# Kernel tuning notes

Hardware: AMD Instinct MI355X
Metric: run time of the kernel (lower is better)

The kernel has to match this reference:

```python
import jax, jax.numpy as jnp
import numpy as np

EPS = 1e-5
K = 9
DILATION = 1

def bn(x, g, b, m, v):
    # x: (B,C,N,1), inference-mode BatchNorm2d with running stats
    sh = (1, -1, 1, 1)
    return (x - m.reshape(sh)) * (g.reshape(sh) / jnp.sqrt(v.reshape(sh) + EPS)) + b.reshape(sh)

def conv1x1(x, w, b):
    # w: (Cout, Cin), x: (B,Cin,N,1)
    return jnp.einsum('oc,bcnj->bonj', w, x) + b.reshape(1, -1, 1, 1)

def knn_idx(feat, k):
    # feat: (B,C,N) -> (B,N,k) indices of k nearest nodes (incl. self)
    xt = jnp.transpose(feat, (0, 2, 1))  # (B,N,C)
    x2 = jnp.sum(xt * xt, axis=-1)       # (B,N)
    dist = x2[:, :, None] - 2.0 * jnp.einsum('bnc,bmc->bnm', xt, xt) + x2[:, None, :]
    _, idx = jax.lax.top_k(-dist, k)
    return idx

def setup_inputs():
    key = jax.random.key(0)
    ks = jax.random.split(key, 24)
    B, C, H, W = 16, 256, 32, 32
    HID = 512
    def g(i, shape, s=1.0):
        return jax.random.normal(ks[i], shape, dtype=jnp.float32) * s
    def pos(i, shape):
        return jax.random.uniform(ks[i], shape, dtype=jnp.float32, minval=0.5, maxval=1.5)
    return {
        'x': g(0, (B, C, H, W)),
        'fc1_w': g(1, (C, C), 0.05), 'fc1_b': g(2, (C,), 0.05),
        'bn1_g': pos(3, (C,)), 'bn1_b': g(4, (C,), 0.1), 'bn1_m': g(5, (C,), 0.1), 'bn1_v': pos(6, (C,)),
        'gc_w': g(7, (HID, 2 * C), 0.05), 'gc_b': g(8, (HID,), 0.05),
        'gbn_g': pos(9, (HID,)), 'gbn_b': g(10, (HID,), 0.1), 'gbn_m': g(11, (HID,), 0.1), 'gbn_v': pos(12, (HID,)),
        'bn2_g': pos(13, (HID,)), 'bn2_b': g(14, (HID,), 0.1), 'bn2_m': g(15, (HID,), 0.1), 'bn2_v': pos(16, (HID,)),
        'fc2_w': g(17, (C, HID), 0.05), 'fc2_b': g(18, (C,), 0.05),
        'bn3_g': pos(19, (C,)), 'bn3_b': g(20, (C,), 0.1), 'bn3_m': g(21, (C,), 0.1), 'bn3_v': pos(22, (C,)),
    }

def reference(x, fc1_w, fc1_b, bn1_g, bn1_b, bn1_m, bn1_v,
              gc_w, gc_b, gbn_g, gbn_b, gbn_m, gbn_v,
              bn2_g, bn2_b, bn2_m, bn2_v,
              fc2_w, fc2_b, bn3_g, bn3_b, bn3_m, bn3_v):
    B, C, H, W = x.shape
    N = H * W
    x = x.reshape(B, C, N, 1)
    shortcut = x
    # fc1: 1x1 conv + BN
    h = bn(conv1x1(x, fc1_w, fc1_b), bn1_g, bn1_b, bn1_m, bn1_v)
    # DyGraphConv2d: dynamic dilated kNN graph over N nodes
    feat = h[..., 0]  # (B,C,N)
    idx = knn_idx(feat, K * DILATION)[:, :, ::DILATION]  # (B,N,K)
    # MRConv2d: max over neighbors of (x_j - x_i)
    x_j = jax.vmap(lambda f, i: f[:, i])(feat, idx)        # (B,C,N,K) gather
    diff_max = jnp.max(x_j - feat[:, :, :, None], axis=-1)  # (B,C,N)
    # interleave [x, max_diff] along channel dim -> (B, 2C, N, 1)
    m = jnp.stack([feat, diff_max], axis=2).reshape(B, 2 * C, N, 1)
    g = conv1x1(m, gc_w, gc_b)
    g = bn(g, gbn_g, gbn_b, gbn_m, gbn_v)  # BasicConv BN, act='None'
    # graph_conv Sequential: BN + GELU (erf, torch default)
    g = jax.nn.gelu(bn(g, bn2_g, bn2_b, bn2_m, bn2_v), approximate=False)
    # fc2 + residual (drop_path=0 -> identity)
    out = bn(conv1x1(g, fc2_w, fc2_b), bn3_g, bn3_b, bn3_m, bn3_v)
    return out + shortcut
```

## Files before the change

kernel.cpp:

```cpp
#include <hip/hip_runtime.h>
#include <hip/hip_bf16.h>
#include <stdint.h>

typedef unsigned long long u64;
typedef __hip_bfloat16 bf16;
typedef short s8v __attribute__((ext_vector_type(8)));
typedef short s4v __attribute__((ext_vector_type(4)));
typedef float f4v __attribute__((ext_vector_type(4)));

#define B_   16
#define C_   256
#define N_   1024
#define HID_ 512

__device__ __forceinline__ unsigned short f2b(float f) {
    unsigned u = __float_as_uint(f);
    unsigned r = (u + 0x7FFFu + ((u >> 16) & 1u)) >> 16;
    return (unsigned short)r;
}
__device__ __forceinline__ float b2f(unsigned short s) {
    return __uint_as_float(((unsigned)s) << 16);
}
__device__ __forceinline__ float ldIn(const void* p, long long i, int bf) {
    return bf ? b2f(((const unsigned short*)p)[i]) : ((const float*)p)[i];
}

__global__ void prep_kernel(const void* xp,
    const void* fc1_b, const void* bn1_g, const void* bn1_b, const void* bn1_m, const void* bn1_v,
    const void* gc_b,  const void* gbn_g, const void* gbn_b, const void* gbn_m, const void* gbn_v,
    const void* bn2_g, const void* bn2_b, const void* bn2_m, const void* bn2_v,
    const void* fc2_b, const void* bn3_g, const void* bn3_b, const void* bn3_m, const void* bn3_v,
    int* flags, float* s1, float* t1, float* Sg, float* Tg, float* s3, float* t3)
{
    __shared__ int sf;
    if (threadIdx.x == 0) {
        const unsigned short* u = (const unsigned short*)xp;
        int cnt = 0;
        for (int i = 0; i < 64; ++i) {
            int e = (u[2 * i] >> 7) & 0xFF;
            cnt += (e >= 87 && e <= 167);
        }
        int f = (cnt >= 48) ? 1 : 0;
        flags[0] = f;
        sf = f;
    }
    __syncthreads();
    int bf = sf;
    int i = threadIdx.x;
    if (i < 256) {
        float g = ldIn(bn1_g, i, bf), bb = ldIn(bn1_b, i, bf);
        float m = ldIn(bn1_m, i, bf), v  = ldIn(bn1_v, i, bf);
        float s = g / sqrtf(v + 1e-5f);
        s1[i] = s;
        t1[i] = (ldIn(fc1_b, i, bf) - m) * s + bb;

        float g3 = ldIn(bn3_g, i, bf), b3 = ldIn(bn3_b, i, bf);
        float m3 = ldIn(bn3_m, i, bf), v3 = ldIn(bn3_v, i, bf);
        float ss3 = g3 / sqrtf(v3 + 1e-5f);
        s3[i] = ss3;
        t3[i] = (ldIn(fc2_b, i, bf) - m3) * ss3 + b3;
    }
    if (i < 512) {
        float gg = ldIn(gbn_g, i, bf), gb = ldIn(gbn_b, i, bf);
        float gm = ldIn(gbn_m, i, bf), gv = ldIn(gbn_v, i, bf);
        float sg = gg / sqrtf(gv + 1e-5f);
        float g2 = ldIn(bn2_g, i, bf), b2 = ldIn(bn2_b, i, bf);
        float m2 = ldIn(bn2_m, i, bf), v2 = ldIn(bn2_v, i, bf);
        float s2 = g2 / sqrtf(v2 + 1e-5f);
        Sg[i] = sg * s2;
        Tg[i] = ((ldIn(gc_b, i, bf) - gm) * sg + gb - m2) * s2 + b2;
    }
}

__global__ __launch_bounds__(256)
void cast_weights(const void* w1, const void* wg, const void* w2,
                  short* W1b, short* Wgb, short* W2b, const int* flags)
{
    int inf = flags[0];
    int i = blockIdx.x * 256 + threadIdx.x;
    if (i < 65536) {
        W1b[i] = (short)f2b(ldIn(w1, i, inf));
    } else if (i < 65536 + 262144) {
        int j = i - 65536;
        Wgb[j] = (short)f2b(ldIn(wg, j, inf));
    } else {
        int j = i - 327680;
        W2b[j] = (short)f2b(ldIn(w2, j, inf));
    }
}

__global__ __launch_bounds__(256)
void fc1_valu(const void* __restrict__ Aw, const void* __restrict__ Bx,
              float* __restrict__ Ft, const float* __restrict__ s1,
              const float* __restrict__ t1, const int* __restrict__ flags)
{
    __shared__ float As[16][68];
    __shared__ float Bs[16][68];

    int inf = flags[0];
    int b  = blockIdx.z;
    int o0 = blockIdx.y * 64, n0 = blockIdx.x * 64;
    int t  = threadIdx.x;
    int tn = t & 15, to = t >> 4;
    long long bbase = (long long)b * C_ * N_;

    float acc[4][4] = {};

    for (int k0 = 0; k0 < C_; k0 += 16) {
        {
            int l = t * 4;
            int ao = l >> 4, ak = l & 15;
            long long ai = (long long)(o0 + ao) * C_ + k0 + ak;
            As[ak + 0][ao] = ldIn(Aw, ai + 0, inf);
            As[ak + 1][ao] = ldIn(Aw, ai + 1, inf);
            As[ak + 2][ao] = ldIn(Aw, ai + 2, inf);
            As[ak + 3][ao] = ldIn(Aw, ai + 3, inf);
        }
        {
            int l = t * 4;
            int bk = l >> 6, bn = l & 63;
            long long bi = bbase + (long long)(k0 + bk) * N_ + n0 + bn;
            Bs[bk][bn + 0] = ldIn(Bx, bi + 0, inf);
            Bs[bk][bn + 1] = ldIn(Bx, bi + 1, inf);
            Bs[bk][bn + 2] = ldIn(Bx, bi + 2, inf);
            Bs[bk][bn + 3] = ldIn(Bx, bi + 3, inf);
        }
        __syncthreads();
        #pragma unroll
        for (int k = 0; k < 16; ++k) {
            float av[4], bv[4];
            #pragma unroll
            for (int i = 0; i < 4; ++i) av[i] = As[k][to * 4 + i];
            #pragma unroll
            for (int j = 0; j < 4; ++j) bv[j] = Bs[k][tn * 4 + j];
            #pragma unroll
            for (int i = 0; i < 4; ++i)
                #pragma unroll
                for (int j = 0; j < 4; ++j) acc[i][j] += av[i] * bv[j];
        }
        __syncthreads();
    }

    #pragma unroll
    for (int i = 0; i < 4; ++i) {
        int o = o0 + to * 4 + i;
        float s = s1[o], tt = t1[o];
        #pragma unroll
        for (int j = 0; j < 4; ++j) {
            int n = n0 + tn * 4 + j;
            Ft[((long long)(b << 10) + n) * C_ + o] = acc[i][j] * s + tt;
        }
    }
}

__global__ __launch_bounds__(256)
void prep_F(const float* __restrict__ Ft, short* __restrict__ Fhi,
            short* __restrict__ Flo, float* __restrict__ x2)
{
    int t = threadIdx.x;
    int wv = t >> 6, lane = t & 63;
    int n = blockIdx.x * 4 + wv;
    int b = blockIdx.y;
    long long base = ((long long)(b << 10) + n) * C_ + lane * 4;
    f4v f = *(const f4v*)(Ft + base);

    s4v hi, lo;
    #pragma unroll
    for (int r = 0; r < 4; ++r) {
        unsigned short h = f2b(f[r]);
        hi[r] = (short)h;
        lo[r] = (short)f2b(f[r] - b2f(h));
    }
    *(s4v*)(Fhi + base) = hi;
    *(s4v*)(Flo + base) = lo;

    float ss = f[0]*f[0] + f[1]*f[1] + f[2]*f[2] + f[3]*f[3];
    #pragma unroll
    for (int s = 32; s >= 1; s >>= 1) ss += __shfl_xor(ss, s, 64);
    if (lane == 0) x2[(b << 10) + n] = ss;
}

__global__ __launch_bounds__(256)
void gram_topk(const short* __restrict__ Fhi, const short* __restrict__ Flo,
               const float* __restrict__ x2, u64* __restrict__ Part)
{
    __shared__ __align__(16) char ldsbuf[37632];
    short* Ah = (short*)(ldsbuf);
    short* Al = (short*)(ldsbuf + 5120);
    short* Bh = (short*)(ldsbuf + 10240);
    short* Bl = (short*)(ldsbuf + 15360);
    float* Dt = (float*)(ldsbuf + 20480);
    u64*   mrg  = (u64*)(ldsbuf);
    u64*   mrg2 = (u64*)(ldsbuf + 20480);

    int t = threadIdx.x;
    int q0 = blockIdx.x * 64, mq = blockIdx.y, b = blockIdx.z;
    int wv = t >> 6, ln = t & 15, quad = (t >> 4) & 3;
    int wq = (wv & 1) * 32, wm = (wv >> 1) * 32;

    u64 l[9];
    #pragma unroll
    for (int i = 0; i < 9; ++i) l[i] = ~0ULL;

    for (int mt = 0; mt < 4; ++mt) {
        int m0 = mq * 256 + mt * 64;
        f4v acc[2][2];
        #pragma unroll
        for (int i = 0; i < 2; ++i)
            #pragma unroll
            for (int j = 0; j < 2; ++j) acc[i][j] = 0.f;

        for (int kc = 0; kc < 8; ++kc) {
            __syncthreads();
            {
                int row = t >> 2, seg = t & 3;
                long long ga = ((long long)((b << 10) + q0 + row)) * C_ + kc * 32 + seg * 8;
                *(s8v*)&Ah[row * 40 + seg * 8] = *(const s8v*)(Fhi + ga);
                *(s8v*)&Al[row * 40 + seg * 8] = *(const s8v*)(Flo + ga);
                long long gb = ((long long)((b << 10) + m0 + row)) * C_ + kc * 32 + seg * 8;
                *(s8v*)&Bh[row * 40 + seg * 8] = *(const s8v*)(Fhi + gb);
                *(s8v*)&Bl[row * 40 + seg * 8] = *(const s8v*)(Flo + gb);
            }
            __syncthreads();
            s8v ah[2], al[2], bh[2], bl[2];
            #pragma unroll
            for (int i = 0; i < 2; ++i) {
                ah[i] = *(s8v*)&Ah[(wq + i * 16 + ln) * 40 + quad * 8];
                al[i] = *(s8v*)&Al[(wq + i * 16 + ln) * 40 + quad * 8];
            }
            #pragma unroll
            for (int j = 0; j < 2; ++j) {
                bh[j] = *(s8v*)&Bh[(wm + j * 16 + ln) * 40 + quad * 8];
                bl[j] = *(s8v*)&Bl[(wm + j * 16 + ln) * 40 + quad * 8];
            }
            #pragma unroll
            for (int i = 0; i < 2; ++i)
                #pragma unroll
                for (int j = 0; j < 2; ++j) {
                    acc[i][j] = __builtin_amdgcn_mfma_f32_16x16x32_bf16(ah[i], bh[j], acc[i][j], 0, 0, 0);
                    acc[i][j] = __builtin_amdgcn_mfma_f32_16x16x32_bf16(ah[i], bl[j], acc[i][j], 0, 0, 0);
                    acc[i][j] = __builtin_amdgcn_mfma_f32_16x16x32_bf16(al[i], bh[j], acc[i][j], 0, 0, 0);
                    acc[i][j] = __builtin_amdgcn_mfma_f32_16x16x32_bf16(al[i], bl[j], acc[i][j], 0, 0, 0);
                }
        }
        __syncthreads();
        #pragma unroll
        for (int j = 0; j < 2; ++j) {
            int ml = wm + j * 16 + ln;
            float xm = x2[(b << 10) + m0 + ml];
            #pragma unroll
            for (int i = 0; i < 2; ++i) {
                #pragma unroll
                for (int r = 0; r < 4; ++r)
                    Dt[(wq + i * 16 + quad * 4 + r) * 67 + ml] = xm - 2.f * acc[i][j][r];
            }
        }
        __syncthreads();
        {
            int row = t >> 2, part = t & 3;
            #pragma unroll
            for (int c = 0; c < 16; ++c) {
                int cc = part * 16 + c;
                float d = Dt[row * 67 + cc];
                int m = m0 + cc;
                unsigned u = __float_as_uint(d);
                u = (u & 0x80000000u) ? ~u : (u | 0x80000000u);
                u64 key = ((u64)u << 32) | (unsigned)m;
                if (key < l[8]) {
                    u64 x = key;
                    #pragma unroll
                    for (int jj = 0; jj < 9; ++jj) {
                        u64 lo2 = l[jj] < x ? l[jj] : x;
                        u64 hi2 = l[jj] < x ? x : l[jj];
                        l[jj] = lo2; x = hi2;
                    }
                }
            }
        }
    }

    __syncthreads();
    {
        int row = t >> 2, part = t & 3;
        #pragma unroll
        for (int k = 0; k < 9; ++k) mrg[(row * 4 + part) * 9 + k] = l[k];
    }
    __syncthreads();
    if (t < 128) {
        int r = t >> 1, pr = t & 1;
        const u64* LA = &mrg[(r * 4 + pr * 2) * 9];
        const u64* LB = LA + 9;
        int ia = 0, ib = 0;
        u64* Po = &mrg2[(r * 2 + pr) * 9];
        #pragma unroll
        for (int k = 0; k < 9; ++k) {
            u64 va = LA[ia], vb = LB[ib];
            bool ta = va < vb;
            Po[k] = ta ? va : vb;
            ia += ta; ib += !ta;
        }
    }
    __syncthreads();
    if (t < 64) {
        const u64* LA = &mrg2[(t * 2) * 9];
        const u64* LB = LA + 9;
        int ia = 0, ib = 0;
        u64* P = Part + (((long long)((b << 10) + q0 + t)) * 4 + mq) * 9;
        #pragma unroll
        for (int k = 0; k < 9; ++k) {
            u64 va = LA[ia], vb = LB[ib];
            bool ta = va < vb;
            P[k] = ta ? va : vb;
            ia += ta; ib += !ta;
        }
    }
}

__global__ __launch_bounds__(256)
void merge_final(const u64* __restrict__ Part, int* __restrict__ ix)
{
    int row = blockIdx.x * 256 + threadIdx.x;
    const u64* L = Part + (long long)row * 36;
    int p0 = 0, p1 = 0, p2 = 0, p3 = 0;
    #pragma unroll
    for (int k = 0; k < 9; ++k) {
        u64 v0 = L[p0], v1 = L[9 + p1], v2 = L[18 + p2], v3 = L[27 + p3];
        u64 m01 = v0 < v1 ? v0 : v1;
        u64 m23 = v2 < v3 ? v2 : v3;
        u64 mn  = m01 < m23 ? m01 : m23;
        ix[row * 9 + k] = (int)(mn & 0xFFFFFFFFu);
        p0 += (mn == v0);
        p1 += (mn == v1) & (mn != v0);
        p2 += (mn == v2) & (mn != v0) & (mn != v1);
        p3 += (mn == v3) & (mn != v0) & (mn != v1) & (mn != v2);
    }
}

__global__ __launch_bounds__(256)
void build_Mt(const float* __restrict__ Ft, const int* __restrict__ idx,
              short* __restrict__ Mt)
{
    int t = threadIdx.x;
    int wv = t >> 6, lane = t & 63;
    int n = blockIdx.x * 4 + wv;
    int b = blockIdx.y;
    int c0 = lane * 4;
    long long nb = (long long)(b << 10) + n;

    f4v f = *(const f4v*)(Ft + nb * C_ + c0);
    const int* id = idx + nb * 9;
    f4v mx = {-3.4e38f, -3.4e38f, -3.4e38f, -3.4e38f};
    #pragma unroll
    for (int k = 0; k < 9; ++k) {
        f4v g = *(const f4v*)(Ft + ((long long)(b << 10) + id[k]) * C_ + c0);
        mx[0] = fmaxf(mx[0], g[0]); mx[1] = fmaxf(mx[1], g[1]);
        mx[2] = fmaxf(mx[2], g[2]); mx[3] = fmaxf(mx[3], g[3]);
    }
    s8v m8;
    #pragma unroll
    for (int r = 0; r < 4; ++r) {
        m8[2 * r]     = (short)f2b(f[r]);
        m8[2 * r + 1] = (short)f2b(mx[r] - f[r]);
    }
    *(s8v*)(Mt + nb * (2 * C_) + 2 * c0) = m8;
}

template<int EPI>
__global__ __launch_bounds__(256)
void mfma_gemm(const short* __restrict__ A, const short* __restrict__ Bm,
               void* __restrict__ Out, const float* __restrict__ scale,
               const float* __restrict__ bias, const void* __restrict__ resid,
               const int* __restrict__ flags, int K, int Odim)
{
    __shared__ short As[128][40];
    __shared__ short Bs[128][40];

    int t = threadIdx.x, b = blockIdx.z;
    int n0 = blockIdx.x * 128, o0 = blockIdx.y * 128;
    int wv = t >> 6, ln = t & 15, quad = (t >> 4) & 3;
    int wo = (wv & 1) * 64, wn = (wv >> 1) * 64;

    f4v acc[4][4];
    #pragma unroll
    for (int i = 0; i < 4; ++i)
        #pragma unroll
        for (int j = 0; j < 4; ++j) acc[i][j] = 0.f;

    const short* Ab = A + (long long)o0 * K;
    const short* Bb = Bm + ((long long)(b << 10) + n0) * K;

    for (int k0 = 0; k0 < K; k0 += 32) {
        __syncthreads();
        #pragma unroll
        for (int s = 0; s < 2; ++s) {
            int sid = t + s * 256;
            int row = sid >> 2, seg = sid & 3;
            *(s8v*)&As[row][seg * 8] = *(const s8v*)(Ab + (long long)row * K + k0 + seg * 8);
            *(s8v*)&Bs[row][seg * 8] = *(const s8v*)(Bb + (long long)row * K + k0 + seg * 8);
        }
        __syncthreads();
        s8v a[4], bf[4];
        #pragma unroll
        for (int i = 0; i < 4; ++i) a[i]  = *(s8v*)&As[wo + i * 16 + ln][quad * 8];
        #pragma unroll
        for (int j = 0; j < 4; ++j) bf[j] = *(s8v*)&Bs[wn + j * 16 + ln][quad * 8];
        #pragma unroll
        for (int i = 0; i < 4; ++i)
            #pragma unroll
            for (int j = 0; j < 4; ++j)
                acc[i][j] = __builtin_amdgcn_mfma_f32_16x16x32_bf16(a[i], bf[j], acc[i][j], 0, 0, 0);
    }

    int inf = flags[0];
    #pragma unroll
    for (int i = 0; i < 4; ++i) {
        int ob = o0 + wo + i * 16 + quad * 4;
        #pragma unroll
        for (int j = 0; j < 4; ++j) {
            int n = n0 + wn + j * 16 + ln;
            f4v v = acc[i][j];
            if (EPI == 0) {
                s4v g;
                #pragma unroll
                for (int r = 0; r < 4; ++r) {
                    float val = v[r] * scale[ob + r] + bias[ob + r];
                    val = 0.5f * val * (1.0f + erff(val * 0.70710678118654752f));
                    g[r] = (short)f2b(val);
                }
                *(s4v*)((short*)Out + ((long long)(b << 10) + n) * Odim + ob) = g;
            } else {
                #pragma unroll
                for (int r = 0; r < 4; ++r) {
                    int o = ob + r;
                    long long oi = ((long long)b * Odim + o) * N_ + n;
                    ((float*)Out)[oi] = v[r] * scale[o] + bias[o] + ldIn(resid, oi, inf);
                }
            }
        }
    }
}

extern "C" void kernel_launch(void* const* d_in, const int* in_sizes, int n_in,
                              void* d_out, int out_size, void* d_ws, size_t ws_size,
                              hipStream_t stream)
{
    const void* p[23];
    if (n_in >= 23 && in_sizes[0] != 4194304 && in_sizes[22] == 4194304) {
        const int amap[23] = {
            22, 13, 12, 1, 0, 2, 3,
            21, 20, 17, 16, 18, 19,
            5, 4, 6, 7,
            15, 14, 9, 8, 10, 11 };
        for (int i = 0; i < 23; ++i) p[i] = d_in[amap[i]];
    } else {
        for (int i = 0; i < 23; ++i) p[i] = d_in[i];
    }

    const void* x     = p[0];
    const void* fc1_w = p[1];
    const void* fc1_b = p[2];
    const void* bn1_g = p[3];
    const void* bn1_b = p[4];
    const void* bn1_m = p[5];
    const void* bn1_v = p[6];
    const void* gc_w  = p[7];
    const void* gc_b  = p[8];
    const void* gbn_g = p[9];
    const void* gbn_b = p[10];
    const void* gbn_m = p[11];
    const void* gbn_v = p[12];
    const void* bn2_g = p[13];
    const void* bn2_b = p[14];
    const void* bn2_m = p[15];
    const void* bn2_v = p[16];
    const void* fc2_w = p[17];
    const void* fc2_b = p[18];
    const void* bn3_g = p[19];
    const void* bn3_b = p[20];
    const void* bn3_m = p[21];
    const void* bn3_v = p[22];

    char* ws = (char*)d_ws;
    size_t off = 0;
    int*   flags = (int*)ws;
    float* s1 = (float*)(ws + 256);
    float* t1 = s1 + 256;
    float* s3 = t1 + 256;
    float* t3 = s3 + 256;
    float* Sg = t3 + 256;
    float* Tg = Sg + 512;
    off = 16384;
    int*   ixAll = (int*)(ws + off);  off += (size_t)B_ * N_ * 9 * 4;
    short* W1b   = (short*)(ws + off); off += (size_t)C_ * C_ * 2;
    short* Wgb   = (short*)(ws + off); off += (size_t)HID_ * 2 * C_ * 2;
    short* W2b   = (short*)(ws + off); off += (size_t)C_ * HID_ * 2;
    float* Ft    = (float*)(ws + off); off += (size_t)B_ * N_ * C_ * 4;
    short* Fhi   = (short*)(ws + off); off += (size_t)B_ * N_ * C_ * 2;
    short* Flo   = (short*)(ws + off); off += (size_t)B_ * N_ * C_ * 2;
    float* x2    = (float*)(ws + off); off += (size_t)B_ * N_ * 4;
    u64*   Part  = (u64*)  (ws + off); off += (size_t)B_ * N_ * 4 * 9 * 8;
    short* Mt    = (short*)(ws + off); off += (size_t)B_ * N_ * 2 * C_ * 2;
    short* Gt    = (short*)(ws + off); off += (size_t)B_ * N_ * HID_ * 2;

    prep_kernel<<<1, 512, 0, stream>>>(x,
        fc1_b, bn1_g, bn1_b, bn1_m, bn1_v,
        gc_b, gbn_g, gbn_b, gbn_m, gbn_v,
        bn2_g, bn2_b, bn2_m, bn2_v,
        fc2_b, bn3_g, bn3_b, bn3_m, bn3_v,
        flags, s1, t1, Sg, Tg, s3, t3);

    cast_weights<<<1792, 256, 0, stream>>>(fc1_w, gc_w, fc2_w,
                                           W1b, Wgb, W2b, flags);

    fc1_valu<<<dim3(16, 4, B_), 256, 0, stream>>>(fc1_w, x, Ft, s1, t1, flags);

    prep_F<<<dim3(N_ / 4, B_), 256, 0, stream>>>(Ft, Fhi, Flo, x2);

    gram_topk<<<dim3(16, 4, 16), 256, 0, stream>>>(Fhi, Flo, x2, Part);
    merge_final<<<64, 256, 0, stream>>>(Part, ixAll);

    build_Mt<<<dim3(256, 16), 256, 0, stream>>>(Ft, ixAll, Mt);

    mfma_gemm<0><<<dim3(8, 4, 16), 256, 0, stream>>>(
        Wgb, Mt, Gt, Sg, Tg, nullptr, flags, 2 * C_, HID_);

    mfma_gemm<1><<<dim3(8, 2, 16), 256, 0, stream>>>(
        W2b, Gt, d_out, s3, t3, x, flags, HID_, C_);
}
```

Before: 326.0 us.

## Restructure gram_topk to keep full 256-candidate accumulators in registers per wave

The gram/top-k kernel now loads all 256 candidate rows (hi and lo) plus the 64 query rows per K-chunk, and each wave owns 16 queries across all 256 candidates with 16 MFMA accumulators held in registers. The per-tile LDS transpose through Dt and the extra syncs are gone, because each lane feeds its accumulator values straight into its running top-9 list. It also drops the lo×lo MFMA term, keeping three of the four bf16 split products. In exchange it uses more LDS and many more VGPRs, which may lower occupancy, and the slightly less precise distances could change neighbor selection at ties.

```diff
diff --git a/kernel.cpp b/kernel.cpp
--- a/kernel.cpp
+++ b/kernel.cpp
@@ -184,96 +184,72 @@
 void gram_topk(const short* __restrict__ Fhi, const short* __restrict__ Flo,
                const float* __restrict__ x2, u64* __restrict__ Part)
 {
-    __shared__ __align__(16) char ldsbuf[37632];
-    short* Ah = (short*)(ldsbuf);
-    short* Al = (short*)(ldsbuf + 5120);
-    short* Bh = (short*)(ldsbuf + 10240);
-    short* Bl = (short*)(ldsbuf + 15360);
-    float* Dt = (float*)(ldsbuf + 20480);
+    __shared__ __align__(16) char ldsbuf[52224];
+    short* Ah  = (short*)(ldsbuf);
+    short* Al  = (short*)(ldsbuf + 20480);
+    short* Bh  = (short*)(ldsbuf + 40960);
+    short* Bl  = (short*)(ldsbuf + 46080);
+    float* x2s = (float*)(ldsbuf + 51200);
     u64*   mrg  = (u64*)(ldsbuf);
     u64*   mrg2 = (u64*)(ldsbuf + 20480);
 
     int t = threadIdx.x;
     int q0 = blockIdx.x * 64, mq = blockIdx.y, b = blockIdx.z;
-    int wv = t >> 6, ln = t & 15, quad = (t >> 4) & 3;
-    int wq = (wv & 1) * 32, wm = (wv >> 1) * 32;
+    int wv = t >> 6, ln15 = t & 15, quad = (t >> 4) & 3;
+
+    x2s[t] = x2[(b << 10) + mq * 256 + t];
+
+    f4v acc[16];
+    #pragma unroll
+    for (int i = 0; i < 16; ++i) acc[i] = 0.f;
+
+    for (int kc = 0; kc < 8; ++kc) {
+        __syncthreads();
+        #pragma unroll
+        for (int s = 0; s < 10; ++s) {
+            int sid = t + s * 256;
+            int row = sid >> 2, seg = sid & 3;
+            const short* src;
+            short* dst;
+            int grow;
+            if (row < 256)      { dst = &Ah[row * 40 + seg * 8];         grow = mq * 256 + row;       src = Fhi; }
+            else if (row < 512) { dst = &Al[(row - 256) * 40 + seg * 8]; grow = mq * 256 + row - 256; src = Flo; }
+            else if (row < 576) { dst = &Bh[(row - 512) * 40 + seg * 8]; grow = q0 + row - 512;       src = Fhi; }
+            else                { dst = &Bl[(row - 576) * 40 + seg * 8]; grow = q0 + row - 576;       src = Flo; }
+            *(s8v*)dst = *(const s8v*)(src + ((long long)((b << 10) + grow)) * C_ + kc * 32 + seg * 8);
+        }
+        __syncthreads();
+        s8v qh = *(s8v*)&Bh[(wv * 16 + ln15) * 40 + quad * 8];
+        s8v ql = *(s8v*)&Bl[(wv * 16 + ln15) * 40 + quad * 8];
+        #pragma unroll
+        for (int i = 0; i < 16; ++i) {
+            s8v mh = *(s8v*)&Ah[(i * 16 + ln15) * 40 + quad * 8];
+            s8v ml = *(s8v*)&Al[(i * 16 + ln15) * 40 + quad * 8];
+            acc[i] = __builtin_amdgcn_mfma_f32_16x16x32_bf16(mh, qh, acc[i], 0, 0, 0);
+            acc[i] = __builtin_amdgcn_mfma_f32_16x16x32_bf16(mh, ql, acc[i], 0, 0, 0);
+            acc[i] = __builtin_amdgcn_mfma_f32_16x16x32_bf16(ml, qh, acc[i], 0, 0, 0);
+        }
+    }
 
     u64 l[9];
     #pragma unroll
     for (int i = 0; i < 9; ++i) l[i] = ~0ULL;
-
-    for (int mt = 0; mt < 4; ++mt) {
-        int m0 = mq * 256 + mt * 64;
-        f4v acc[2][2];
-        #pragma unroll
-        for (int i = 0; i < 2; ++i)
-            #pragma unroll
-            for (int j = 0; j < 2; ++j) acc[i][j] = 0.f;
-
-        for (int kc = 0; kc < 8; ++kc) {
-            __syncthreads();
-            {
-                int row = t >> 2, seg = t & 3;
-                long long ga = ((long long)((b << 10) + q0 + row)) * C_ + kc * 32 + seg * 8;
-                *(s8v*)&Ah[row * 40 + seg * 8] = *(const s8v*)(Fhi + ga);
-                *(s8v*)&Al[row * 40 + seg * 8] = *(const s8v*)(Flo + ga);
-                long long gb = ((long long)((b << 10) + m0 + row)) * C_ + kc * 32 + seg * 8;
-                *(s8v*)&Bh[row * 40 + seg * 8] = *(const s8v*)(Fhi + gb);
-                *(s8v*)&Bl[row * 40 + seg * 8] = *(const s8v*)(Flo + gb);
-            }
-            __syncthreads();
-            s8v ah[2], al[2], bh[2], bl[2];
-            #pragma unroll
-            for (int i = 0; i < 2; ++i) {
-                ah[i] = *(s8v*)&Ah[(wq + i * 16 + ln) * 40 + quad * 8];
-                al[i] = *(s8v*)&Al[(wq + i * 16 + ln) * 40 + quad * 8];
-            }
-            #pragma unroll
-            for (int j = 0; j < 2; ++j) {
-                bh[j] = *(s8v*)&Bh[(wm + j * 16 + ln) * 40 + quad * 8];
-                bl[j] = *(s8v*)&Bl[(wm + j * 16 + ln) * 40 + quad * 8];
-            }
-            #pragma unroll
-            for (int i = 0; i < 2; ++i)
+    #pragma unroll
+    for (int i = 0; i < 16; ++i) {
+        #pragma unroll
+        for (int r = 0; r < 4; ++r) {
+            int mloc = i * 16 + quad * 4 + r;
+            float d = x2s[mloc] - 2.f * acc[i][r];
+            unsigned u = __float_as_uint(d);
+            u = (u & 0x80000000u) ? ~u : (u | 0x80000000u);
+            u64 key = ((u64)u << 32) | (unsigned)(mq * 256 + mloc);
+            if (key < l[8]) {
+                u64 x = key;
                 #pragma unroll
-                for (int j = 0; j < 2; ++j) {
-                    acc[i][j] = __builtin_amdgcn_mfma_f32_16x16x32_bf16(ah[i], bh[j], acc[i][j], 0, 0, 0);
-                    acc[i][j] = __builtin_amdgcn_mfma_f32_16x16x32_bf16(ah[i], bl[j], acc[i][j], 0, 0, 0);
-                    acc[i][j] = __builtin_amdgcn_mfma_f32_16x16x32_bf16(al[i], bh[j], acc[i][j], 0, 0, 0);
-                    acc[i][j] = __builtin_amdgcn_mfma_f32_16x16x32_bf16(al[i], bl[j], acc[i][j], 0, 0, 0);
-                }
-        }
-        __syncthreads();
-        #pragma unroll
-        for (int j = 0; j < 2; ++j) {
-            int ml = wm + j * 16 + ln;
-            float xm = x2[(b << 10) + m0 + ml];
-            #pragma unroll
-            for (int i = 0; i < 2; ++i) {
-                #pragma unroll
-                for (int r = 0; r < 4; ++r)
-                    Dt[(wq + i * 16 + quad * 4 + r) * 67 + ml] = xm - 2.f * acc[i][j][r];
-            }
-        }
-        __syncthreads();
-        {
-            int row = t >> 2, part = t & 3;
-            #pragma unroll
-            for (int c = 0; c < 16; ++c) {
-                int cc = part * 16 + c;
-                float d = Dt[row * 67 + cc];
-                int m = m0 + cc;
-                unsigned u = __float_as_uint(d);
-                u = (u & 0x80000000u) ? ~u : (u | 0x80000000u);
-                u64 key = ((u64)u << 32) | (unsigned)m;
-                if (key < l[8]) {
-                    u64 x = key;
-                    #pragma unroll
-                    for (int jj = 0; jj < 9; ++jj) {
-                        u64 lo2 = l[jj] < x ? l[jj] : x;
-                        u64 hi2 = l[jj] < x ? x : l[jj];
-                        l[jj] = lo2; x = hi2;
-                    }
+                for (int jj = 0; jj < 9; ++jj) {
+                    u64 lo2 = l[jj] < x ? l[jj] : x;
+                    u64 hi2 = l[jj] < x ? x : l[jj];
+                    l[jj] = lo2; x = hi2;
                 }
             }
         }
@@ -281,9 +257,9 @@
 
     __syncthreads();
     {
-        int row = t >> 2, part = t & 3;
-        #pragma unroll
-        for (int k = 0; k < 9; ++k) mrg[(row * 4 + part) * 9 + k] = l[k];
+        int qloc = wv * 16 + ln15;
+        #pragma unroll
+        for (int k = 0; k < 9; ++k) mrg[(qloc * 4 + quad) * 9 + k] = l[k];
     }
     __syncthreads();
     if (t < 128) {
```

Result: no change. 330.0 us (+1.2%).
